# Kernel optimization log

Measured on AMD Instinct MI355X. Metric: run time of the kernel, lower is better.

Reference implementation:

```python
import jax, jax.numpy as jnp
import numpy as np

LAMBDA_A = 1.0
NUM_ITER = 3
K = 64
BN_EPS = 1e-5


def setup_inputs() -> dict:
    key = jax.random.key(0)
    ks = jax.random.split(key, 8)
    B, C, H, W = 16, 512, 64, 64
    x = jax.random.normal(ks[0], (B, C, H, W), dtype=jnp.float32)
    # codebook mu: init normal(std~sqrt(2/k)) then L2-normalize along dim=1 (k axis), as in torch init
    mu = jax.random.normal(ks[1], (C, K), dtype=jnp.float32) * np.sqrt(2.0 / K)
    mu = mu / jnp.maximum(jnp.linalg.norm(mu, axis=1, keepdims=True), 1e-12)
    # 1x1 convs expressed as (out, in) matrices
    stem_w = jax.random.normal(ks[2], (C, C), dtype=jnp.float32) * np.sqrt(2.0 / C)
    stem_b = jnp.zeros((C,), dtype=jnp.float32)
    head_w = jax.random.normal(ks[3], (C, C), dtype=jnp.float32) * np.sqrt(2.0 / C)
    head_b = jnp.zeros((C,), dtype=jnp.float32)
    bn_gamma = jnp.ones((C,), dtype=jnp.float32)
    bn_beta = jnp.zeros((C,), dtype=jnp.float32)
    return {"x": x, "mu": mu, "stem_w": stem_w, "stem_b": stem_b,
            "head_w": head_w, "head_b": head_b,
            "bn_gamma": bn_gamma, "bn_beta": bn_beta}


def _conv1x1(x, w, b):
    # x: (B,C,H,W), w: (O,C)
    return jnp.einsum('bchw,oc->bohw', x, w) + b[None, :, None, None]


def reference(x, mu, stem_w, stem_b, head_w, head_b, bn_gamma, bn_beta):
    B, C, H, W = x.shape
    N = H * W
    y = _conv1x1(x, stem_w, stem_b)                 # (B,C,H,W)
    yf = y.reshape(B, C, N).transpose(0, 2, 1)      # (B,N,C)

    mu_b = jnp.broadcast_to(mu[None], (B, C, K))    # (B,C,K)
    z = None
    for _ in range(NUM_ITER):
        z = jax.nn.softmax(LAMBDA_A * jnp.einsum('bnc,bck->bnk', yf, mu_b), axis=2)
        zn = z / (1e-6 + z.sum(axis=1, keepdims=True))
        mu_b = jnp.einsum('bnc,bnk->bck', yf, zn)
        mu_b = mu_b / jnp.maximum(jnp.linalg.norm(mu_b, axis=1, keepdims=True), 1e-12)

    # EM loop runs under no_grad in torch
    mu_b = jax.lax.stop_gradient(mu_b)
    z = jax.lax.stop_gradient(z)

    y2 = jnp.einsum('bck,bnk->bcn', mu_b, z).reshape(B, C, H, W)

    # head: ReLU -> 1x1 conv -> BatchNorm2d (training-mode batch stats)
    h = _conv1x1(jnp.maximum(y2, 0.0), head_w, head_b)
    mean = h.mean(axis=(0, 2, 3), keepdims=True)
    var = h.var(axis=(0, 2, 3), keepdims=True)
    h = (h - mean) * jax.lax.rsqrt(var + BN_EPS)
    h = h * bn_gamma[None, :, None, None] + bn_beta[None, :, None, None]

    return jnp.maximum(h + x, 0.0)
```

## Files before the change

kernel.cpp:

```cpp
#include <hip/hip_runtime.h>


typedef _Float16 half_t;
typedef _Float16 half4 __attribute__((ext_vector_type(4)));
typedef _Float16 half8 __attribute__((ext_vector_type(8)));
typedef float f32x4 __attribute__((ext_vector_type(4)));

#define GLD_LDS(gp, lp) __builtin_amdgcn_global_load_lds( \
    (const __attribute__((address_space(1))) void*)(gp),  \
    (__attribute__((address_space(3))) void*)(lp), 16, 0, 0)

#define SBAR __builtin_amdgcn_sched_barrier(0)
#define RAWBAR do { SBAR; __builtin_amdgcn_s_barrier(); SBAR; } while (0)
#define LGKM0 do { asm volatile("s_waitcnt lgkmcnt(0)" ::: "memory"); SBAR; } while (0)

template <int L> __device__ __forceinline__ void vmwait() {
  if constexpr (L == 8) asm volatile("s_waitcnt vmcnt(8)" ::: "memory");
  else if constexpr (L == 6) asm volatile("s_waitcnt vmcnt(6)" ::: "memory");
  else if constexpr (L == 4) asm volatile("s_waitcnt vmcnt(4)" ::: "memory");
  else asm volatile("s_waitcnt vmcnt(0)" ::: "memory");
}

constexpr int CB = 16;
constexpr int CC = 512;
constexpr int CN = 4096;
constexpr int CKK = 64;
constexpr long MALL = (long)CB * CN;

__device__ inline int swz8(int bid, int n) {
  return (bid & 7) * (n >> 3) + (bid >> 3);
}

__global__ __launch_bounds__(256) void prep(
    const float* __restrict__ stem_w, const float* __restrict__ head_w,
    const float* __restrict__ mu,
    half_t* __restrict__ swh, half_t* __restrict__ hwh,
    half_t* __restrict__ muT, half_t* __restrict__ muck)
{
  int i = blockIdx.x * 256 + threadIdx.x;
  swh[i] = (half_t)stem_w[i];
  hwh[i] = (half_t)head_w[i];
  if (i < CC * CKK) {
    int c = i >> 6, k = i & 63;
    half_t v = (half_t)mu[i];
    for (int b = 0; b < CB; ++b) {
      muT[(long)b * CKK * CC + (long)k * CC + c] = v;
      muck[(long)b * CC * CKK + i] = v;
    }
  }
}

template <bool SWZ>
__global__ __launch_bounds__(256) void gemm_stem(
    const float* __restrict__ X, const half_t* __restrict__ Bw,
    const float* __restrict__ bias,
    half_t* __restrict__ Co, half_t* __restrict__ CoT)
{
  constexpr int SAB = 16384;
  __shared__ __align__(16) half_t smem[2 * SAB];
  const int tid = threadIdx.x, wid = tid >> 6, lane = tid & 63;
  int bid = blockIdx.x;
  if constexpr (SWZ) bid = swz8(bid, gridDim.x);
  const int tm = bid >> 2, tn = bid & 3;
  const long row0 = (long)tm * 128;
  const long b = row0 >> 12;
  const int n0 = (int)(row0 & 4095);
  const float* Xb = X + b * ((long)CC * CN) + n0;
  const half_t* Bb = Bw + (long)tn * 128 * CC;
  const int wr = wid >> 1, wc = wid & 1;

  const int an = tid & 127;
  const int ac0 = (tid >> 7) * 32;
  const int r8 = lane >> 3;
  const int gcs = ((lane & 7) ^ r8) * 8;

  float va[32];
  auto issueA = [&](int ks) {
    const float* p = Xb + (long)(ks * 64 + ac0) * CN + an;
#pragma unroll
    for (int e = 0; e < 32; ++e) va[e] = p[(long)e * CN];
  };
  auto writeA = [&](int buf) {
    half_t* dA = smem + buf * SAB;
#pragma unroll
    for (int g = 0; g < 4; ++g) {
      half8 h;
#pragma unroll
      for (int e = 0; e < 8; ++e) h[e] = (half_t)va[g * 8 + e];
      const int chunk = (ac0 >> 3) + g;
      *(half8*)&dA[an * 64 + ((chunk ^ (an & 7)) << 3)] = h;
    }
  };
  auto stageB = [&](int ks, int buf) {
    half_t* dB = smem + buf * SAB + 8192;
    const half_t* gb = Bb + (long)ks * 64;
#pragma unroll
    for (int c = wid; c < 16; c += 4)
      GLD_LDS(gb + (long)(c * 8 + r8) * CC + gcs, &dB[c * 512]);
  };

  f32x4 acc[4][4];
#pragma unroll
  for (int i = 0; i < 4; ++i)
#pragma unroll
    for (int j = 0; j < 4; ++j) acc[i][j] = f32x4{0.f, 0.f, 0.f, 0.f};

  issueA(0);
  stageB(0, 0);
  vmwait<0>();
  writeA(0);
  LGKM0;
  RAWBAR;

  int cur = 0;
  for (int ks = 0; ks < 8; ++ks) {
    if (ks < 7) { issueA(ks + 1); stageB(ks + 1, cur ^ 1); }
    const half_t* lA = smem + cur * SAB;
    const half_t* lB = lA + 8192;
#pragma unroll
    for (int kk = 0; kk < 2; ++kk) {
      half8 af[4], bfr[4];
      const int cg = kk * 4 + (lane >> 4);
#pragma unroll
      for (int i = 0; i < 4; ++i) {
        const int rA = wr * 64 + i * 16 + (lane & 15);
        af[i] = *(const half8*)&lA[rA * 64 + ((cg ^ (rA & 7)) << 3)];
      }
#pragma unroll
      for (int j = 0; j < 4; ++j) {
        const int rB = wc * 64 + j * 16 + (lane & 15);
        bfr[j] = *(const half8*)&lB[rB * 64 + ((cg ^ (rB & 7)) << 3)];
      }
      __builtin_amdgcn_s_setprio(1);
#pragma unroll
      for (int i = 0; i < 4; ++i)
#pragma unroll
        for (int j = 0; j < 4; ++j)
          acc[i][j] = __builtin_amdgcn_mfma_f32_16x16x32_f16(af[i], bfr[j],
                                                             acc[i][j], 0, 0, 0);
      __builtin_amdgcn_s_setprio(0);
    }
    RAWBAR;
    if (ks < 7) {
      vmwait<0>();
      writeA(cur ^ 1);
      LGKM0;
    }
    RAWBAR;
    cur ^= 1;
  }

  constexpr int PIT = 132;
  half_t* ep = smem;
#pragma unroll
  for (int j = 0; j < 4; ++j) {
    const int nl = wc * 64 + j * 16 + (lane & 15);
    const float bv = bias[tn * 128 + nl];
#pragma unroll
    for (int i = 0; i < 4; ++i) {
      const int ml = wr * 64 + i * 16 + ((lane >> 4) << 2);
      half4 h;
#pragma unroll
      for (int r = 0; r < 4; ++r) h[r] = (half_t)(acc[i][j][r] + bv);
      *(half4*)&ep[nl * PIT + ml] = h;
    }
  }
  __syncthreads();
  {
#pragma unroll
    for (int s = 0; s < 8; ++s) {
      const int q = tid + 256 * s;
      const int m = q & 127, cc8 = q >> 7;
      half8 v;
#pragma unroll
      for (int e = 0; e < 8; ++e) v[e] = ep[(cc8 * 8 + e) * PIT + m];
      *(half8*)&Co[(row0 + m) * CC + tn * 128 + cc8 * 8] = v;
    }
  }
  {
#pragma unroll
    for (int s = 0; s < 8; ++s) {
      const int q = tid + 256 * s;
      const int mc = q & 15, cl = q >> 4;
      half8 v = *(const half8*)&ep[cl * PIT + mc * 8];
      *(half8*)&CoT[(b * CC + tn * 128 + cl) * CN + n0 + mc * 8] = v;
    }
  }
}

template <int BM, int BN, int MODE, int EPI, bool SWZ>
__global__ __launch_bounds__(256) void gemm_abt(
    const half_t* __restrict__ A, const half_t* __restrict__ Bm,
    half_t* __restrict__ Co, half_t* __restrict__ CoT,
    float* __restrict__ Cacc, const float* __restrict__ bias,
    int M, int Nn, int Kk, int ksplit, long sA, long sB, long sC)
{
  constexpr int FM = BM / 32, FN = BN / 32;
  constexpr int HB = (BM + BN) * 64;
  constexpr int LCNT = (BM / 8) / 4 + (BN / 8) / 4;
  constexpr int STG = 2 * HB;
  constexpr int EPS = (EPI != 0) ? BN * (BM + 4) : 0;
  constexpr int TOT = STG > EPS ? STG : EPS;
  __shared__ __align__(16) half_t smem[TOT];

  const int tid = threadIdx.x, wid = tid >> 6, lane = tid & 63;
  int bid = blockIdx.x;
  if constexpr (SWZ) bid = swz8(bid, gridDim.x);
  const int tilesN = Nn / BN;
  const int tm = bid / tilesN, tn = bid % tilesN;
  const long bz = blockIdx.z;
  const half_t* Ab = A + bz * sA + (long)tm * BM * Kk;
  const half_t* Bb = Bm + bz * sB + (long)tn * BN * Kk;
  const int ksteps = Kk >> 6;
  const int per = ksteps / ksplit;
  const int ks0 = blockIdx.y * per, ks1 = ks0 + per;
  const int wr = wid >> 1, wc = wid & 1;

  const int r8 = lane >> 3;
  const int gcs = ((lane & 7) ^ r8) * 8;

  auto stage = [&](int ks, int buf) {
    half_t* dA = smem + buf * HB;
    half_t* dB = dA + BM * 64;
    const half_t* ga = Ab + (long)ks * 64;
#pragma unroll
    for (int c = wid; c < BM / 8; c += 4)
      GLD_LDS(ga + (long)(c * 8 + r8) * Kk + gcs, &dA[c * 512]);
    const half_t* gb = Bb + (long)ks * 64;
#pragma unroll
    for (int c = wid; c < BN / 8; c += 4)
      GLD_LDS(gb + (long)(c * 8 + r8) * Kk + gcs, &dB[c * 512]);
  };

  f32x4 acc[FM][FN];
#pragma unroll
  for (int i = 0; i < FM; ++i)
#pragma unroll
    for (int j = 0; j < FN; ++j) acc[i][j] = f32x4{0.f, 0.f, 0.f, 0.f};

  stage(ks0, 0);
  if (ks0 + 1 < ks1) { stage(ks0 + 1, 1); vmwait<LCNT>(); }
  else               { vmwait<0>(); }
  RAWBAR;

  int cur = 0;
  for (int ks = ks0; ks < ks1; ++ks) {
    const half_t* lA = smem + cur * HB;
    const half_t* lB = lA + BM * 64;
#pragma unroll
    for (int kk = 0; kk < 2; ++kk) {
      half8 af[FM], bfr[FN];
      const int cg = kk * 4 + (lane >> 4);
#pragma unroll
      for (int i = 0; i < FM; ++i) {
        const int rA = wr * (BM / 2) + i * 16 + (lane & 15);
        af[i] = *(const half8*)&lA[rA * 64 + ((cg ^ (rA & 7)) << 3)];
      }
#pragma unroll
      for (int j = 0; j < FN; ++j) {
        const int rB = wc * (BN / 2) + j * 16 + (lane & 15);
        bfr[j] = *(const half8*)&lB[rB * 64 + ((cg ^ (rB & 7)) << 3)];
      }
      __builtin_amdgcn_s_setprio(1);
#pragma unroll
      for (int i = 0; i < FM; ++i)
#pragma unroll
        for (int j = 0; j < FN; ++j)
          acc[i][j] = __builtin_amdgcn_mfma_f32_16x16x32_f16(af[i], bfr[j],
                                                             acc[i][j], 0, 0, 0);
      __builtin_amdgcn_s_setprio(0);
    }
    RAWBAR;
    const bool more = (ks + 2 < ks1);
    if (more) { stage(ks + 2, cur); vmwait<LCNT>(); }
    else      { vmwait<0>(); }
    RAWBAR;
    cur ^= 1;
  }

  if constexpr (EPI != 0) {
    static_assert(BM == 128 && BN == 128, "LDS epilogue assumes 128x128");
    constexpr int PIT = BM + 4;
    half_t* ep = smem;
#pragma unroll
    for (int j = 0; j < FN; ++j) {
      const int nl = wc * 64 + j * 16 + (lane & 15);
      float bv = 0.f;
      if constexpr (MODE & 1) bv = bias[tn * BN + nl];
#pragma unroll
      for (int i = 0; i < FM; ++i) {
        const int ml = wr * 64 + i * 16 + ((lane >> 4) << 2);
        half4 h;
#pragma unroll
        for (int r = 0; r < 4; ++r) {
          float v = acc[i][j][r] + bv;
          if constexpr (MODE & 2) v = fmaxf(v, 0.f);
          h[r] = (half_t)v;
        }
        *(half4*)&ep[nl * PIT + ml] = h;
      }
    }
    __syncthreads();
    const long rowbase = (long)tm * BM;
    if constexpr (EPI & 1) {
#pragma unroll
      for (int s = 0; s < 8; ++s) {
        const int q = tid + 256 * s;
        const int m = q & 127, cc8 = q >> 7;
        half8 v;
#pragma unroll
        for (int e = 0; e < 8; ++e) v[e] = ep[(cc8 * 8 + e) * PIT + m];
        *(half8*)&Co[bz * sC + (rowbase + m) * Nn + tn * BN + cc8 * 8] = v;
      }
    }
    if constexpr (EPI & 2) {
      const long b = rowbase >> 12, nbase = rowbase & 4095;
#pragma unroll
      for (int s = 0; s < 8; ++s) {
        const int q = tid + 256 * s;
        const int mc = q & 15, cl = q >> 4;
        half8 v = *(const half8*)&ep[cl * PIT + mc * 8];
        *(half8*)&CoT[(b * Nn + tn * BN + cl) * 4096 + nbase + mc * 8] = v;
      }
    }
  } else {
#pragma unroll
    for (int j = 0; j < FN; ++j) {
      const int n = tn * BN + wc * (BN / 2) + j * 16 + (lane & 15);
      float bv = 0.f;
      if constexpr (MODE & 1) bv = bias[n];
#pragma unroll
      for (int i = 0; i < FM; ++i) {
        const int mbase = tm * BM + wr * (BM / 2) + i * 16 + ((lane >> 4) << 2);
#pragma unroll
        for (int r = 0; r < 4; ++r) {
          const long idx = bz * sC + (long)(mbase + r) * Nn + n;
          if constexpr ((MODE & 4) != 0) {
            atomicAdd(&Cacc[idx], acc[i][j][r]);
          } else {
            float v = acc[i][j][r] + bv;
            if constexpr ((MODE & 2) != 0) v = fmaxf(v, 0.f);
            Co[idx] = (half_t)v;
          }
        }
      }
    }
  }
}

__global__ __launch_bounds__(256) void s_softmax(
    const half_t* __restrict__ Yf, const half_t* __restrict__ muT,
    half_t* __restrict__ zp, half_t* __restrict__ zT)
{
  constexpr int HB = (128 + 64) * 64;
  __shared__ __align__(16) union {
    half_t st[2 * HB];
    half_t zh[128 * 68];
  } sm;
  const int tid = threadIdx.x, wid = tid >> 6, lane = tid & 63;
  const int tm = blockIdx.x;
  const long bz = blockIdx.z;
  const half_t* Ab = Yf + bz * (long)CN * CC + (long)tm * 128 * CC;
  const half_t* Bb = muT + bz * (long)CKK * CC;

  const int r8 = lane >> 3;
  const int gcs = ((lane & 7) ^ r8) * 8;

  auto stage = [&](int ks, int buf) {
    half_t* dA = sm.st + buf * HB;
    half_t* dB = dA + 128 * 64;
    const half_t* ga = Ab + (long)ks * 64;
#pragma unroll
    for (int c = wid; c < 16; c += 4)
      GLD_LDS(ga + (long)(c * 8 + r8) * CC + gcs, &dA[c * 512]);
    const half_t* gb = Bb + (long)ks * 64;
#pragma unroll
    for (int c = wid; c < 8; c += 4)
      GLD_LDS(gb + (long)(c * 8 + r8) * CC + gcs, &dB[c * 512]);
  };

  f32x4 acc[2][4];
#pragma unroll
  for (int i = 0; i < 2; ++i)
#pragma unroll
    for (int j = 0; j < 4; ++j) acc[i][j] = f32x4{0.f, 0.f, 0.f, 0.f};

  stage(0, 0);
  stage(1, 1);
  vmwait<6>();
  RAWBAR;
  int cur = 0;
  for (int ks = 0; ks < 8; ++ks) {
    const half_t* lA = sm.st + cur * HB;
    const half_t* lB = lA + 128 * 64;
#pragma unroll
    for (int kk = 0; kk < 2; ++kk) {
      half8 af[2], bfr[4];
      const int cg = kk * 4 + (lane >> 4);
#pragma unroll
      for (int i = 0; i < 2; ++i) {
        const int rA = wid * 32 + i * 16 + (lane & 15);
        af[i] = *(const half8*)&lA[rA * 64 + ((cg ^ (rA & 7)) << 3)];
      }
#pragma unroll
      for (int j = 0; j < 4; ++j) {
        const int rB = j * 16 + (lane & 15);
        bfr[j] = *(const half8*)&lB[rB * 64 + ((cg ^ (rB & 7)) << 3)];
      }
      __builtin_amdgcn_s_setprio(1);
#pragma unroll
      for (int i = 0; i < 2; ++i)
#pragma unroll
        for (int j = 0; j < 4; ++j)
          acc[i][j] = __builtin_amdgcn_mfma_f32_16x16x32_f16(af[i], bfr[j],
                                                             acc[i][j], 0, 0, 0);
      __builtin_amdgcn_s_setprio(0);
    }
    RAWBAR;
    const bool more = (ks + 2 < 8);
    if (more) { stage(ks + 2, cur); vmwait<6>(); }
    else      { vmwait<0>(); }
    RAWBAR;
    cur ^= 1;
  }

#pragma unroll
  for (int i = 0; i < 2; ++i)
#pragma unroll
    for (int r = 0; r < 4; ++r) {
      float mx = fmaxf(fmaxf(acc[i][0][r], acc[i][1][r]),
                       fmaxf(acc[i][2][r], acc[i][3][r]));
#pragma unroll
      for (int m = 1; m < 16; m <<= 1) mx = fmaxf(mx, __shfl_xor(mx, m));
      float p[4], s = 0.f;
#pragma unroll
      for (int j = 0; j < 4; ++j) { p[j] = __expf(acc[i][j][r] - mx); s += p[j]; }
#pragma unroll
      for (int m = 1; m < 16; m <<= 1) s += __shfl_xor(s, m);
      const float inv = 1.f / s;
#pragma unroll
      for (int j = 0; j < 4; ++j) acc[i][j][r] = p[j] * inv;
    }

#pragma unroll
  for (int i = 0; i < 2; ++i)
#pragma unroll
    for (int j = 0; j < 4; ++j)
#pragma unroll
      for (int r = 0; r < 4; ++r) {
        const int row = wid * 32 + i * 16 + ((lane >> 4) << 2) + r;
        const int col = j * 16 + (lane & 15);
        sm.zh[row * 68 + col] = (half_t)acc[i][j][r];
      }
  __syncthreads();
  if (zp) {
    const int nl = tid >> 1, seg = tid & 1;
    const long base = bz * (long)CN * CKK + (long)(tm * 128 + nl) * CKK + seg * 32;
#pragma unroll
    for (int g = 0; g < 4; ++g) {
      half8 v;
#pragma unroll
      for (int e = 0; e < 8; ++e) v[e] = sm.zh[nl * 68 + seg * 32 + g * 8 + e];
      *(half8*)&zp[base + g * 8] = v;
    }
  }
  {
    const int k = tid >> 2, seg = tid & 3;
    const long base = bz * (long)CKK * CN + (long)k * CN + tm * 128 + seg * 32;
#pragma unroll
    for (int g = 0; g < 4; ++g) {
      half8 v;
#pragma unroll
      for (int e = 0; e < 8; ++e) v[e] = sm.zh[(seg * 32 + g * 8 + e) * 68 + k];
      *(half8*)&zT[base + g * 8] = v;
    }
  }
}

__global__ __launch_bounds__(64) void mu_norm(
    const float* __restrict__ acc, half_t* __restrict__ muT, half_t* __restrict__ muck)
{
  const int bk = blockIdx.x;
  const int b = bk >> 6, k = bk & 63;
  const float* row = acc + (long)bk * CC;
  const int t = threadIdx.x;
  float v[8]; float s = 0.f;
#pragma unroll
  for (int e = 0; e < 8; ++e) { v[e] = row[t * 8 + e]; s += v[e] * v[e]; }
#pragma unroll
  for (int m = 1; m < 64; m <<= 1) s += __shfl_xor(s, m);
  const float inv = 1.f / fmaxf(sqrtf(s), 1e-12f);
  half8 o;
#pragma unroll
  for (int e = 0; e < 8; ++e) o[e] = (half_t)(v[e] * inv);
  *(half8*)&muT[(long)bk * CC + t * 8] = o;
  half_t* mc = muck + (long)b * CC * CKK;
#pragma unroll
  for (int e = 0; e < 8; ++e) mc[(long)(t * 8 + e) * CKK + k] = o[e];
}

__global__ __launch_bounds__(256) void bn_stats2(
    const half_t* __restrict__ hcn, float* __restrict__ stats)
{
  const int c = blockIdx.x, tid = threadIdx.x;
  float s = 0.f, s2 = 0.f;
  for (int b = 0; b < CB; ++b) {
    const half_t* p = hcn + ((long)b * CC + c) * CN;
    for (int i = tid * 8; i < CN; i += 2048) {
      half8 v = *(const half8*)&p[i];
#pragma unroll
      for (int e = 0; e < 8; ++e) { float f = (float)v[e]; s += f; s2 += f * f; }
    }
  }
#pragma unroll
  for (int m = 1; m < 64; m <<= 1) { s += __shfl_xor(s, m); s2 += __shfl_xor(s2, m); }
  __shared__ float r[8];
  const int wid = tid >> 6;
  if ((tid & 63) == 0) { r[wid] = s; r[4 + wid] = s2; }
  __syncthreads();
  if (tid == 0) {
    stats[c] = r[0] + r[1] + r[2] + r[3];
    stats[CC + c] = r[4] + r[5] + r[6] + r[7];
  }
}

__global__ void bn_param(const float* __restrict__ stats,
                         const float* __restrict__ gamma, const float* __restrict__ beta,
                         float* __restrict__ scsh)
{
  const int c = threadIdx.x;
  const float cnt = 1.f / 65536.f;
  const float mean = stats[c] * cnt;
  const float var = stats[CC + c] * cnt - mean * mean;
  const float sc = gamma[c] * rsqrtf(var + 1e-5f);
  scsh[c] = sc;
  scsh[CC + c] = beta[c] - mean * sc;
}

__global__ __launch_bounds__(256) void bn_final2(
    const half_t* __restrict__ hcn, const float* __restrict__ x,
    const float* __restrict__ scsh, float* __restrict__ out)
{
  const long i8 = (long)blockIdx.x * 256 + threadIdx.x;
  const int c = (int)((i8 >> 9) & 511);
  const float sc = scsh[c], sh = scsh[CC + c];
  half8 h = *(const half8*)&hcn[i8 * 8];
  f32x4 x0 = *(const f32x4*)&x[i8 * 8];
  f32x4 x1 = *(const f32x4*)&x[i8 * 8 + 4];
  f32x4 o0, o1;
#pragma unroll
  for (int e = 0; e < 4; ++e) o0[e] = fmaxf((float)h[e] * sc + sh + x0[e], 0.f);
#pragma unroll
  for (int e = 0; e < 4; ++e) o1[e] = fmaxf((float)h[4 + e] * sc + sh + x1[e], 0.f);
  *(f32x4*)&out[i8 * 8] = o0;
  *(f32x4*)&out[i8 * 8 + 4] = o1;
}

extern "C" void kernel_launch(void* const* d_in, const int* in_sizes, int n_in,
                              void* d_out, int out_size, void* d_ws, size_t ws_size,
                              hipStream_t stream)
{
  const float* x      = (const float*)d_in[0];
  const float* mu     = (const float*)d_in[1];
  const float* stem_w = (const float*)d_in[2];
  const float* stem_b = (const float*)d_in[3];
  const float* head_w = (const float*)d_in[4];
  const float* head_b = (const float*)d_in[5];
  const float* bn_g   = (const float*)d_in[6];
  const float* bn_b   = (const float*)d_in[7];
  float* out = (float*)d_out;

  const size_t NEED = 214ull << 20;
  if (ws_size < NEED) {
    hipMemsetAsync(d_out, 0, (size_t)out_size * 4, stream);
    return;
  }
  char* ws = (char*)d_ws;
  const long MB = 1 << 20;
  half_t* y2f  = (half_t*)(ws);
  half_t* Yf   = (half_t*)(ws + 64 * MB);
  half_t* ycn  = (half_t*)(ws + 128 * MB);
  half_t* z    = (half_t*)(ws + 192 * MB);
  half_t* zT   = (half_t*)(ws + 200 * MB);
  half_t* muT  = (half_t*)(ws + 208 * MB);
  half_t* muck = (half_t*)(ws + 209 * MB);
  float* muacc = (float*)(ws + 210 * MB);
  half_t* swh  = (half_t*)(ws + 212 * MB);
  half_t* hwh  = (half_t*)(ws + 212 * MB + 512 * 1024);
  float* stats = (float*)(ws + 213 * MB);
  float* scsh  = (float*)(ws + 213 * MB + 8 * 1024);
  half_t* hcn = Yf;

  prep<<<1024, 256, 0, stream>>>(stem_w, head_w, mu, swh, hwh, muT, muck);
  gemm_stem<true><<<2048, 256, 0, stream>>>(x, swh, stem_b, Yf, ycn);

  for (int it = 0; it < 3; ++it) {
    s_softmax<<<dim3(32, 1, 16), 256, 0, stream>>>(
        Yf, muT, (it == 2) ? z : nullptr, zT);
    hipMemsetAsync(muacc, 0, (size_t)CB * CKK * CC * 4, stream);
    gemm_abt<64, 128, 4, 0, false><<<dim3(4, 4, 16), 256, 0, stream>>>(
        zT, ycn, nullptr, nullptr, muacc, nullptr, CKK, CC, CN, 4,
        (long)CKK * CN, (long)CC * CN, (long)CKK * CC);
    mu_norm<<<CB * CKK, 64, 0, stream>>>(muacc, muT, muck);
  }
  gemm_abt<128, 128, 2, 1, true><<<dim3(128, 1, 16), 256, 0, stream>>>(
      z, muck, y2f, nullptr, nullptr, nullptr, CN, CC, CKK, 1,
      (long)CN * CKK, (long)CC * CKK, (long)CN * CC);
  gemm_abt<128, 128, 1, 2, true><<<dim3(2048, 1, 1), 256, 0, stream>>>(
      y2f, hwh, nullptr, hcn, nullptr, head_b, (int)MALL, CC, CC, 1, 0, 0, 0);

  bn_stats2<<<CC, 256, 0, stream>>>(hcn, stats);
  bn_param<<<1, 512, 0, stream>>>(stats, bn_g, bn_b, scsh);
  bn_final2<<<16384, 256, 0, stream>>>(hcn, x, scsh, out);
}
```

Baseline: 400.6 us.

## Replace double-buffered LDS prefetch with single-buffer load-then-compute loops

Removes the two-stage double-buffered LDS pipeline from the stem GEMM, the generic A·Bᵀ GEMM and the softmax GEMM. Each k-step now loads into a single LDS buffer, waits for all global loads, then computes. This halves shared-memory use, which may allow more resident blocks per CU. In exchange, global-load latency is no longer overlapped with MFMA work inside a block.

```diff
diff --git a/kernel.cpp b/kernel.cpp
--- a/kernel.cpp
+++ b/kernel.cpp
@@ -13,13 +13,7 @@
 #define SBAR __builtin_amdgcn_sched_barrier(0)
 #define RAWBAR do { SBAR; __builtin_amdgcn_s_barrier(); SBAR; } while (0)
 #define LGKM0 do { asm volatile("s_waitcnt lgkmcnt(0)" ::: "memory"); SBAR; } while (0)
-
-template <int L> __device__ __forceinline__ void vmwait() {
-  if constexpr (L == 8) asm volatile("s_waitcnt vmcnt(8)" ::: "memory");
-  else if constexpr (L == 6) asm volatile("s_waitcnt vmcnt(6)" ::: "memory");
-  else if constexpr (L == 4) asm volatile("s_waitcnt vmcnt(4)" ::: "memory");
-  else asm volatile("s_waitcnt vmcnt(0)" ::: "memory");
-}
+#define VM0   do { asm volatile("s_waitcnt vmcnt(0)" ::: "memory"); SBAR; } while (0)
 
 constexpr int CB = 16;
 constexpr int CC = 512;
@@ -56,8 +50,7 @@
     const float* __restrict__ bias,
     half_t* __restrict__ Co, half_t* __restrict__ CoT)
 {
-  constexpr int SAB = 16384;
-  __shared__ __align__(16) half_t smem[2 * SAB];
+  __shared__ __align__(16) half_t smem[16896];
   const int tid = threadIdx.x, wid = tid >> 6, lane = tid & 63;
   int bid = blockIdx.x;
   if constexpr (SWZ) bid = swz8(bid, gridDim.x);
@@ -80,8 +73,8 @@
 #pragma unroll
     for (int e = 0; e < 32; ++e) va[e] = p[(long)e * CN];
   };
-  auto writeA = [&](int buf) {
-    half_t* dA = smem + buf * SAB;
+  auto writeA = [&]() {
+    half_t* dA = smem;
 #pragma unroll
     for (int g = 0; g < 4; ++g) {
       half8 h;
@@ -91,8 +84,8 @@
       *(half8*)&dA[an * 64 + ((chunk ^ (an & 7)) << 3)] = h;
     }
   };
-  auto stageB = [&](int ks, int buf) {
-    half_t* dB = smem + buf * SAB + 8192;
+  auto stageB = [&](int ks) {
+    half_t* dB = smem + 8192;
     const half_t* gb = Bb + (long)ks * 64;
 #pragma unroll
     for (int c = wid; c < 16; c += 4)
@@ -106,17 +99,15 @@
     for (int j = 0; j < 4; ++j) acc[i][j] = f32x4{0.f, 0.f, 0.f, 0.f};
 
   issueA(0);
-  stageB(0, 0);
-  vmwait<0>();
-  writeA(0);
-  LGKM0;
-  RAWBAR;
-
-  int cur = 0;
   for (int ks = 0; ks < 8; ++ks) {
-    if (ks < 7) { issueA(ks + 1); stageB(ks + 1, cur ^ 1); }
-    const half_t* lA = smem + cur * SAB;
-    const half_t* lB = lA + 8192;
+    stageB(ks);
+    VM0;
+    writeA();
+    if (ks < 7) issueA(ks + 1);
+    LGKM0;
+    RAWBAR;
+    const half_t* lA = smem;
+    const half_t* lB = smem + 8192;
 #pragma unroll
     for (int kk = 0; kk < 2; ++kk) {
       half8 af[4], bfr[4];
@@ -141,13 +132,6 @@
       __builtin_amdgcn_s_setprio(0);
     }
     RAWBAR;
-    if (ks < 7) {
-      vmwait<0>();
-      writeA(cur ^ 1);
-      LGKM0;
-    }
-    RAWBAR;
-    cur ^= 1;
   }
 
   constexpr int PIT = 132;
@@ -197,10 +181,8 @@
 {
   constexpr int FM = BM / 32, FN = BN / 32;
   constexpr int HB = (BM + BN) * 64;
-  constexpr int LCNT = (BM / 8) / 4 + (BN / 8) / 4;
-  constexpr int STG = 2 * HB;
   constexpr int EPS = (EPI != 0) ? BN * (BM + 4) : 0;
-  constexpr int TOT = STG > EPS ? STG : EPS;
+  constexpr int TOT = HB > EPS ? HB : EPS;
   __shared__ __align__(16) half_t smem[TOT];
 
   const int tid = threadIdx.x, wid = tid >> 6, lane = tid & 63;
@@ -219,9 +201,9 @@
   const int r8 = lane >> 3;
   const int gcs = ((lane & 7) ^ r8) * 8;
 
-  auto stage = [&](int ks, int buf) {
-    half_t* dA = smem + buf * HB;
-    half_t* dB = dA + BM * 64;
+  auto stage = [&](int ks) {
+    half_t* dA = smem;
+    half_t* dB = smem + BM * 64;
     const half_t* ga = Ab + (long)ks * 64;
 #pragma unroll
     for (int c = wid; c < BM / 8; c += 4)
@@ -238,15 +220,12 @@
 #pragma unroll
     for (int j = 0; j < FN; ++j) acc[i][j] = f32x4{0.f, 0.f, 0.f, 0.f};
 
-  stage(ks0, 0);
-  if (ks0 + 1 < ks1) { stage(ks0 + 1, 1); vmwait<LCNT>(); }
-  else               { vmwait<0>(); }
-  RAWBAR;
-
-  int cur = 0;
   for (int ks = ks0; ks < ks1; ++ks) {
-    const half_t* lA = smem + cur * HB;
-    const half_t* lB = lA + BM * 64;
+    stage(ks);
+    VM0;
+    RAWBAR;
+    const half_t* lA = smem;
+    const half_t* lB = smem + BM * 64;
 #pragma unroll
     for (int kk = 0; kk < 2; ++kk) {
       half8 af[FM], bfr[FN];
@@ -271,11 +250,6 @@
       __builtin_amdgcn_s_setprio(0);
     }
     RAWBAR;
-    const bool more = (ks + 2 < ks1);
-    if (more) { stage(ks + 2, cur); vmwait<LCNT>(); }
-    else      { vmwait<0>(); }
-    RAWBAR;
-    cur ^= 1;
   }
 
   if constexpr (EPI != 0) {
@@ -354,7 +328,7 @@
 {
   constexpr int HB = (128 + 64) * 64;
   __shared__ __align__(16) union {
-    half_t st[2 * HB];
+    half_t st[HB];
     half_t zh[128 * 68];
   } sm;
   const int tid = threadIdx.x, wid = tid >> 6, lane = tid & 63;
@@ -366,9 +340,9 @@
   const int r8 = lane >> 3;
   const int gcs = ((lane & 7) ^ r8) * 8;
 
-  auto stage = [&](int ks, int buf) {
-    half_t* dA = sm.st + buf * HB;
-    half_t* dB = dA + 128 * 64;
+  auto stage = [&](int ks) {
+    half_t* dA = sm.st;
+    half_t* dB = sm.st + 128 * 64;
     const half_t* ga = Ab + (long)ks * 64;
 #pragma unroll
     for (int c = wid; c < 16; c += 4)
@@ -385,14 +359,12 @@
 #pragma unroll
     for (int j = 0; j < 4; ++j) acc[i][j] = f32x4{0.f, 0.f, 0.f, 0.f};
 
-  stage(0, 0);
-  stage(1, 1);
-  vmwait<6>();
-  RAWBAR;
-  int cur = 0;
   for (int ks = 0; ks < 8; ++ks) {
-    const half_t* lA = sm.st + cur * HB;
-    const half_t* lB = lA + 128 * 64;
+    stage(ks);
+    VM0;
+    RAWBAR;
+    const half_t* lA = sm.st;
+    const half_t* lB = sm.st + 128 * 64;
 #pragma unroll
     for (int kk = 0; kk < 2; ++kk) {
       half8 af[2], bfr[4];
@@ -417,11 +389,6 @@
       __builtin_amdgcn_s_setprio(0);
     }
     RAWBAR;
-    const bool more = (ks + 2 < 8);
-    if (more) { stage(ks + 2, cur); vmwait<6>(); }
-    else      { vmwait<0>(); }
-    RAWBAR;
-    cur ^= 1;
   }
 
 #pragma unroll
```

After: 407.4 us. No clear change (+1.7%).

## Fuse BN statistics into head GEMM epilogue and drop split-K atomics

Applied to the files above, without the earlier changes.

The head GEMM epilogue now accumulates per-channel sum and sum-of-squares and atomically adds them to a stats buffer. This removes the separate bn_stats2 pass that re-read the whole fp16 activation tensor. Separately, the split-K mu GEMM now writes each partial slice to its own buffer instead of using atomicAdd into a zeroed buffer, and mu_norm sums the four slices. That also removes the per-iteration memset. The costs are many float atomics on 1024 stats entries, and statistics taken from fp32 values before fp16 rounding, which is slightly different numerically.

```diff
diff --git a/kernel.cpp b/kernel.cpp
--- a/kernel.cpp
+++ b/kernel.cpp
@@ -188,11 +188,12 @@
   }
 }
 
-template <int BM, int BN, int MODE, int EPI, bool SWZ>
+template <int BM, int BN, int MODE, int EPI, bool SWZ, bool STATS>
 __global__ __launch_bounds__(256) void gemm_abt(
     const half_t* __restrict__ A, const half_t* __restrict__ Bm,
     half_t* __restrict__ Co, half_t* __restrict__ CoT,
     float* __restrict__ Cacc, const float* __restrict__ bias,
+    float* __restrict__ stats,
     int M, int Nn, int Kk, int ksplit, long sA, long sB, long sC)
 {
   constexpr int FM = BM / 32, FN = BN / 32;
@@ -287,6 +288,7 @@
       const int nl = wc * 64 + j * 16 + (lane & 15);
       float bv = 0.f;
       if constexpr (MODE & 1) bv = bias[tn * BN + nl];
+      float s1 = 0.f, s2 = 0.f;
 #pragma unroll
       for (int i = 0; i < FM; ++i) {
         const int ml = wr * 64 + i * 16 + ((lane >> 4) << 2);
@@ -295,9 +297,19 @@
         for (int r = 0; r < 4; ++r) {
           float v = acc[i][j][r] + bv;
           if constexpr (MODE & 2) v = fmaxf(v, 0.f);
+          if constexpr (STATS) { s1 += v; s2 += v * v; }
           h[r] = (half_t)v;
         }
         *(half4*)&ep[nl * PIT + ml] = h;
+      }
+      if constexpr (STATS) {
+        s1 += __shfl_xor(s1, 16); s1 += __shfl_xor(s1, 32);
+        s2 += __shfl_xor(s2, 16); s2 += __shfl_xor(s2, 32);
+        if (lane < 16) {
+          const int ch = tn * BN + nl;
+          atomicAdd(&stats[ch], s1);
+          atomicAdd(&stats[CC + ch], s2);
+        }
       }
     }
     __syncthreads();
@@ -334,10 +346,12 @@
         const int mbase = tm * BM + wr * (BM / 2) + i * 16 + ((lane >> 4) << 2);
 #pragma unroll
         for (int r = 0; r < 4; ++r) {
-          const long idx = bz * sC + (long)(mbase + r) * Nn + n;
           if constexpr ((MODE & 4) != 0) {
-            atomicAdd(&Cacc[idx], acc[i][j][r]);
+            const long idx = bz * sC + (long)blockIdx.y * ((long)BM * Nn) +
+                             (long)(mbase + r) * Nn + n;
+            Cacc[idx] = acc[i][j][r];
           } else {
+            const long idx = bz * sC + (long)(mbase + r) * Nn + n;
             float v = acc[i][j][r] + bv;
             if constexpr ((MODE & 2) != 0) v = fmaxf(v, 0.f);
             Co[idx] = (half_t)v;
@@ -482,11 +496,15 @@
 {
   const int bk = blockIdx.x;
   const int b = bk >> 6, k = bk & 63;
-  const float* row = acc + (long)bk * CC;
+  const float* base = acc + ((long)b * 4 * CKK + k) * CC;
   const int t = threadIdx.x;
   float v[8]; float s = 0.f;
 #pragma unroll
-  for (int e = 0; e < 8; ++e) { v[e] = row[t * 8 + e]; s += v[e] * v[e]; }
+  for (int e = 0; e < 8; ++e) {
+    float a = base[t * 8 + e] + base[CKK * CC + t * 8 + e] +
+              base[2 * CKK * CC + t * 8 + e] + base[3 * CKK * CC + t * 8 + e];
+    v[e] = a; s += a * a;
+  }
 #pragma unroll
   for (int m = 1; m < 64; m <<= 1) s += __shfl_xor(s, m);
   const float inv = 1.f / fmaxf(sqrtf(s), 1e-12f);
@@ -497,31 +515,6 @@
   half_t* mc = muck + (long)b * CC * CKK;
 #pragma unroll
   for (int e = 0; e < 8; ++e) mc[(long)(t * 8 + e) * CKK + k] = o[e];
-}
-
-__global__ __launch_bounds__(256) void bn_stats2(
-    const half_t* __restrict__ hcn, float* __restrict__ stats)
-{
-  const int c = blockIdx.x, tid = threadIdx.x;
-  float s = 0.f, s2 = 0.f;
-  for (int b = 0; b < CB; ++b) {
-    const half_t* p = hcn + ((long)b * CC + c) * CN;
-    for (int i = tid * 8; i < CN; i += 2048) {
-      half8 v = *(const half8*)&p[i];
-#pragma unroll
-      for (int e = 0; e < 8; ++e) { float f = (float)v[e]; s += f; s2 += f * f; }
-    }
-  }
-#pragma unroll
-  for (int m = 1; m < 64; m <<= 1) { s += __shfl_xor(s, m); s2 += __shfl_xor(s2, m); }
-  __shared__ float r[8];
-  const int wid = tid >> 6;
-  if ((tid & 63) == 0) { r[wid] = s; r[4 + wid] = s2; }
-  __syncthreads();
-  if (tid == 0) {
-    stats[c] = r[0] + r[1] + r[2] + r[3];
-    stats[CC + c] = r[4] + r[5] + r[6] + r[7];
-  }
 }
 
 __global__ void bn_param(const float* __restrict__ stats,
@@ -578,13 +571,13 @@
   char* ws = (char*)d_ws;
   const long MB = 1 << 20;
   half_t* y2f  = (half_t*)(ws);
+  float* muacc = (float*)(ws);
   half_t* Yf   = (half_t*)(ws + 64 * MB);
   half_t* ycn  = (half_t*)(ws + 128 * MB);
   half_t* z    = (half_t*)(ws + 192 * MB);
   half_t* zT   = (half_t*)(ws + 200 * MB);
   half_t* muT  = (half_t*)(ws + 208 * MB);
   half_t* muck = (half_t*)(ws + 209 * MB);
-  float* muacc = (float*)(ws + 210 * MB);
   half_t* swh  = (half_t*)(ws + 212 * MB);
   half_t* hwh  = (half_t*)(ws + 212 * MB + 512 * 1024);
   float* stats = (float*)(ws + 213 * MB);
@@ -597,19 +590,18 @@
   for (int it = 0; it < 3; ++it) {
     s_softmax<<<dim3(32, 1, 16), 256, 0, stream>>>(
         Yf, muT, (it == 2) ? z : nullptr, zT);
-    hipMemsetAsync(muacc, 0, (size_t)CB * CKK * CC * 4, stream);
-    gemm_abt<64, 128, 4, 0, false><<<dim3(4, 4, 16), 256, 0, stream>>>(
-        zT, ycn, nullptr, nullptr, muacc, nullptr, CKK, CC, CN, 4,
-        (long)CKK * CN, (long)CC * CN, (long)CKK * CC);
+    gemm_abt<64, 128, 4, 0, false, false><<<dim3(4, 4, 16), 256, 0, stream>>>(
+        zT, ycn, nullptr, nullptr, muacc, nullptr, nullptr, CKK, CC, CN, 4,
+        (long)CKK * CN, (long)CC * CN, (long)4 * CKK * CC);
     mu_norm<<<CB * CKK, 64, 0, stream>>>(muacc, muT, muck);
   }
-  gemm_abt<128, 128, 2, 1, true><<<dim3(128, 1, 16), 256, 0, stream>>>(
-      z, muck, y2f, nullptr, nullptr, nullptr, CN, CC, CKK, 1,
+  gemm_abt<128, 128, 2, 1, true, false><<<dim3(128, 1, 16), 256, 0, stream>>>(
+      z, muck, y2f, nullptr, nullptr, nullptr, nullptr, CN, CC, CKK, 1,
       (long)CN * CKK, (long)CC * CKK, (long)CN * CC);
-  gemm_abt<128, 128, 1, 2, true><<<dim3(2048, 1, 1), 256, 0, stream>>>(
-      y2f, hwh, nullptr, hcn, nullptr, head_b, (int)MALL, CC, CC, 1, 0, 0, 0);
-
-  bn_stats2<<<CC, 256, 0, stream>>>(hcn, stats);
+  hipMemsetAsync(stats, 0, 2 * CC * sizeof(float), stream);
+  gemm_abt<128, 128, 1, 2, true, true><<<dim3(2048, 1, 1), 256, 0, stream>>>(
+      y2f, hwh, nullptr, hcn, nullptr, head_b, stats, (int)MALL, CC, CC, 1, 0, 0, 0);
+
   bn_param<<<1, 512, 0, stream>>>(stats, bn_g, bn_b, scsh);
   bn_final2<<<16384, 256, 0, stream>>>(hcn, x, scsh, out);
 }
```

Result: faster. 383.4 us (-4.3%).
